# Kernel optimization log

Hardware: AMD Instinct MI355X
Metric: run time of the kernel (lower is better)

## Reference

```python
import jax, jax.numpy as jnp
from jax import lax
import numpy as np

B, C, T = 128, 64, 750
NOUT, K, HID = 4, 16, 128


def _conv(x, w, b=None):
    y = lax.conv_general_dilated(x, w, (1, 1), 'VALID', dimension_numbers=('NCHW', 'OIHW', 'NCHW'))
    return y if b is None else y + b[None, :, None, None]


def _bn(x, g, b, m, v):
    s = g / jnp.sqrt(v + 1e-5)
    return (x - m[None, :, None, None]) * s[None, :, None, None] + b[None, :, None, None]


def _pool(x):
    return lax.reduce_window(x, -jnp.inf, lax.max, (1, 1, 3, 1), (1, 1, 3, 1), 'VALID')


def _backbone(x, ct_w, ct_b, cs_w, bn1, c2_w, bn2, c3_w, bn3, c4_w, bn4, fc_w, fc_b):
    # x: (B, C, T) -> (B, 1, T, C)  (braindecode transpose_time_to_spat)
    h = jnp.transpose(x, (0, 2, 1))[:, None]
    h = _conv(h, ct_w, ct_b)              # (B,25,T-9,C)
    h = _conv(h, cs_w)                    # (B,25,T-9,1)
    h = _pool(jax.nn.elu(_bn(h, *bn1)))   # (B,25,247,1)
    h = _pool(jax.nn.elu(_bn(_conv(h, c2_w), *bn2)))  # (B,50,79,1)
    h = _pool(jax.nn.elu(_bn(_conv(h, c3_w), *bn3)))  # (B,100,23,1)
    h = _pool(jax.nn.elu(_bn(_conv(h, c4_w), *bn4)))  # (B,200,4,1)
    h = _conv(h, fc_w, fc_b)              # (B,NOUT,1,1)
    return h[:, :, 0, 0]                  # (B,NOUT)


def _heads(feats, cluster_ids, hW1, hb1, hW2, hb2):
    # gather per-sample head params, batched small GEMMs (MoE-style dispatch)
    h = jax.nn.relu(jnp.einsum('bf,bfh->bh', feats, hW1[cluster_ids]) + hb1[cluster_ids])
    return jnp.einsum('bh,bho->bo', h, hW2[cluster_ids]) + hb2[cluster_ids]


def setup_inputs() -> dict:
    key = jax.random.key(0)
    ks = jax.random.split(key, 40)
    n = lambda i, shape, s=0.1: jax.random.normal(ks[i], shape, dtype=jnp.float32) * s
    u = lambda i, shape: jax.random.uniform(ks[i], shape, dtype=jnp.float32) + 0.5
    inp = {
        'x': n(0, (B, C, T), 1.0),
        'cluster_ids': jax.random.randint(ks[1], (B,), 0, K),
        'ct_w': n(2, (25, 1, 10, 1)), 'ct_b': n(3, (25,)),
        'cs_w': n(4, (25, 25, 1, C)),
        'bn1_g': u(5, (25,)), 'bn1_b': n(6, (25,)), 'bn1_m': n(7, (25,)), 'bn1_v': u(8, (25,)),
        'c2_w': n(9, (50, 25, 10, 1)),
        'bn2_g': u(10, (50,)), 'bn2_b': n(11, (50,)), 'bn2_m': n(12, (50,)), 'bn2_v': u(13, (50,)),
        'c3_w': n(14, (100, 50, 10, 1)),
        'bn3_g': u(15, (100,)), 'bn3_b': n(16, (100,)), 'bn3_m': n(17, (100,)), 'bn3_v': u(18, (100,)),
        'c4_w': n(19, (200, 100, 10, 1)),
        'bn4_g': u(20, (200,)), 'bn4_b': n(21, (200,)), 'bn4_m': n(22, (200,)), 'bn4_v': u(23, (200,)),
        'fc_w': n(24, (NOUT, 200, 4, 1)), 'fc_b': n(25, (NOUT,)),
        'hW1': n(26, (K, NOUT, HID)), 'hb1': n(27, (K, HID)),
        'hW2': n(28, (K, HID, NOUT)), 'hb2': n(29, (K, NOUT)),
    }
    return inp


def reference(x, cluster_ids, ct_w, ct_b, cs_w,
              bn1_g, bn1_b, bn1_m, bn1_v, c2_w,
              bn2_g, bn2_b, bn2_m, bn2_v, c3_w,
              bn3_g, bn3_b, bn3_m, bn3_v, c4_w,
              bn4_g, bn4_b, bn4_m, bn4_v, fc_w, fc_b,
              hW1, hb1, hW2, hb2):
    feats = _backbone(x, ct_w, ct_b, cs_w,
                      (bn1_g, bn1_b, bn1_m, bn1_v), c2_w,
                      (bn2_g, bn2_b, bn2_m, bn2_v), c3_w,
                      (bn3_g, bn3_b, bn3_m, bn3_v), c4_w,
                      (bn4_g, bn4_b, bn4_m, bn4_v), fc_w, fc_b)
    return _heads(feats, cluster_ids, hW1, hb1, hW2, hb2)
```

## Files before the change

kernel.cpp:

```cpp
#include <hip/hip_runtime.h>
#include <hip/hip_bf16.h>
#include <math.h>

typedef __attribute__((ext_vector_type(8))) short short8v;
typedef __attribute__((ext_vector_type(4))) float f32x4;

#define F_S1 0
#define F_H1 32
#define F_S2 64
#define F_H2 128
#define F_S3 192
#define F_H3 320
#define F_S4 448
#define F_H4 704
#define F_B1 960
#define F_END 1024
#define H_BASE (F_END*2)
#define H_P1  H_BASE
#define H_WA1 (H_P1 + 128*8192)
#define H_WA2 (H_WA1 + 32*640)
#define H_WA3 (H_WA2 + 64*320)
#define H_WA4 (H_WA3 + 112*640)

#define N_WA1 (32*640)
#define N_WA2 (64*320)
#define N_WA3 (112*640)
#define N_WA4 (208*1280)
#define N_WTOT (N_WA1 + N_WA2 + N_WA3 + N_WA4)

__device__ __forceinline__ float eluf(float v) {
    return v > 0.f ? v : (expf(v) - 1.f);
}
__device__ __forceinline__ float ldh(const __hip_bfloat16* p) { return __bfloat162float(*p); }

__device__ __forceinline__ void ld4f(const float* p, float* v) {
    float2 a = *(const float2*)p, c = *(const float2*)(p + 2);
    v[0] = a.x; v[1] = a.y; v[2] = c.x; v[3] = c.y;
}

__global__ __launch_bounds__(256) void k_pre2(
    const float* __restrict__ ct_w, const float* __restrict__ ct_b,
    const float* __restrict__ cs_w,
    const float* __restrict__ g1, const float* __restrict__ b1,
    const float* __restrict__ m1, const float* __restrict__ v1,
    const float* __restrict__ w2,
    const float* __restrict__ g2, const float* __restrict__ b2,
    const float* __restrict__ m2, const float* __restrict__ v2,
    const float* __restrict__ w3,
    const float* __restrict__ g3, const float* __restrict__ b3,
    const float* __restrict__ m3, const float* __restrict__ v3,
    const float* __restrict__ w4,
    const float* __restrict__ g4, const float* __restrict__ b4,
    const float* __restrict__ m4, const float* __restrict__ v4,
    float* __restrict__ ws) {
    __hip_bfloat16* wsh = (__hip_bfloat16*)ws;
    int t = blockIdx.x * 256 + threadIdx.x;
    if (t < N_WA1) {
        int o = t / 640, kv = t - o * 640, kk = kv / 64, c = kv - kk * 64;
        float s = 0.f;
        if (o < 25)
            for (int i = 0; i < 25; ++i)
                s += cs_w[(o * 25 + i) * 64 + c] * ct_w[i * 10 + kk];
        wsh[H_WA1 + t] = __float2bfloat16(s);
    } else if (t < N_WA1 + N_WA2) {
        int u = t - N_WA1;
        int o = u / 320, kv = u - o * 320, kk = kv / 32, c = kv - kk * 32;
        float s = (o < 50 && c < 25) ? w2[(o * 25 + c) * 10 + kk] : 0.f;
        wsh[H_WA2 + u] = __float2bfloat16(s);
    } else if (t < N_WA1 + N_WA2 + N_WA3) {
        int u = t - N_WA1 - N_WA2;
        int o = u / 640, kv = u - o * 640, kk = kv / 64, c = kv - kk * 64;
        float s = (o < 100 && c < 50) ? w3[(o * 50 + c) * 10 + kk] : 0.f;
        wsh[H_WA3 + u] = __float2bfloat16(s);
    } else if (t < N_WTOT) {
        int u = t - N_WA1 - N_WA2 - N_WA3;
        int o = u / 1280, kv = u - o * 1280, kk = kv / 128, c = kv - kk * 128;
        float s = (o < 200 && c < 100) ? w4[(o * 100 + c) * 10 + kk] : 0.f;
        wsh[H_WA4 + u] = __float2bfloat16(s);
    } else {
        int j = t - N_WTOT;
        if (j < 25) {
            float sc = g1[j] / sqrtf(v1[j] + 1e-5f);
            ws[F_S1 + j] = sc; ws[F_H1 + j] = b1[j] - m1[j] * sc;
        } else if (j >= 32 && j < 82) {
            int ch = j - 32;
            float sc = g2[ch] / sqrtf(v2[ch] + 1e-5f);
            ws[F_S2 + ch] = sc; ws[F_H2 + ch] = b2[ch] - m2[ch] * sc;
        } else if (j >= 96 && j < 196) {
            int ch = j - 96;
            float sc = g3[ch] / sqrtf(v3[ch] + 1e-5f);
            ws[F_S3 + ch] = sc; ws[F_H3 + ch] = b3[ch] - m3[ch] * sc;
        } else if (j >= 224 && j < 424) {
            int ch = j - 224;
            float sc = g4[ch] / sqrtf(v4[ch] + 1e-5f);
            ws[F_S4 + ch] = sc; ws[F_H4 + ch] = b4[ch] - m4[ch] * sc;
        } else if (j >= 448 && j < 473) {
            int o = j - 448;
            float s = 0.f;
            for (int i = 0; i < 25; ++i) {
                float cs = 0.f;
                for (int c = 0; c < 64; ++c) cs += cs_w[(o * 25 + i) * 64 + c];
                s += cs * ct_b[i];
            }
            ws[F_B1 + o] = s;
        }
    }
}

template<int NS, int CB, int CINP>
__device__ __forceinline__ f32x4 conv_item(
    const __hip_bfloat16* __restrict__ Wrow,
    const __hip_bfloat16* xb, int lo, int kg, int rowBase) {
    constexpr int SWM = (CINP >= 64) ? 7 : 3;
    const short8v* Ap = (const short8v*)Wrow;
    f32x4 acc = {0.f, 0.f, 0.f, 0.f};
#pragma unroll 1
    for (int sb = 0; sb < NS; sb += 10) {
        short8v af[10];
#pragma unroll
        for (int u = 0; u < 10; ++u) af[u] = Ap[(sb + u) * 4 + kg];
#pragma unroll
        for (int u = 0; u < 10; ++u) {
            int s = sb + u;
            int kk = s / CB, cb = s % CB;
            int r = rowBase + lo + kk;
            int cs = (cb * 32 + kg * 8) ^ (8 * (r & SWM));
            short8v bf = *(const short8v*)&xb[r * CINP + cs];
            acc = __builtin_amdgcn_mfma_f32_16x16x32_bf16(af[u], bf, acc, 0, 0, 0);
        }
    }
    return acc;
}

__global__ __launch_bounds__(256) void k_conv1(
    const float* __restrict__ x, float* __restrict__ ws) {
    __hip_bfloat16* wsh = (__hip_bfloat16*)ws;
    const __hip_bfloat16* Wa = wsh + H_WA1;
    int bx = blockIdx.x, b = blockIdx.y;
    int tp0 = bx * 42;
    int PTb = min(42, 247 - tp0);
    int t0 = 126 * bx;

    __shared__ __align__(16) __hip_bfloat16 xb[144 * 64];
    __shared__ __align__(16) __hip_bfloat16 eb[32 * 128];

    for (int f = threadIdx.x; f < 64 * 36; f += 256) {
        int c = f / 36, j = f - c * 36;
        int t = t0 + 4 * j;
        const float* src = x + ((size_t)b * 64 + c) * 750 + t;
        float v[4];
        if (t + 3 < 750) {
            ld4f(src, v);
        } else {
#pragma unroll
            for (int e = 0; e < 4; ++e) v[e] = (t + e < 750) ? src[e] : 0.f;
        }
#pragma unroll
        for (int e = 0; e < 4; ++e) {
            int r = 4 * j + e;
            xb[r * 64 + (c ^ (8 * (r & 7)))] = __float2bfloat16(v[e]);
        }
    }
    __syncthreads();

    int lane = threadIdx.x & 63, wid = threadIdx.x >> 6;
    int lo = lane & 15, kg = lane >> 4;
    int ot = wid >> 1, ctg = wid & 1;
    const short8v* Ap = (const short8v*)(Wa + (size_t)(ot * 16 + lo) * 640);
    f32x4 acc[4];
#pragma unroll
    for (int q = 0; q < 4; ++q) acc[q] = (f32x4){0.f, 0.f, 0.f, 0.f};
#pragma unroll 1
    for (int sb = 0; sb < 20; sb += 10) {
        short8v af[10];
#pragma unroll
        for (int u = 0; u < 10; ++u) af[u] = Ap[(sb + u) * 4 + kg];
#pragma unroll
        for (int u = 0; u < 10; ++u) {
            int s = sb + u;
            int kk = s >> 1, cb = s & 1;
#pragma unroll
            for (int q = 0; q < 4; ++q) {
                int r = (ctg * 4 + q) * 16 + lo + kk;
                int cs = (cb * 32 + kg * 8) ^ (8 * (r & 7));
                short8v bf = *(const short8v*)&xb[r * 64 + cs];
                acc[q] = __builtin_amdgcn_mfma_f32_16x16x32_bf16(af[u], bf, acc[q], 0, 0, 0);
            }
        }
    }
#pragma unroll
    for (int q = 0; q < 4; ++q) {
        int tloc = (ctg * 4 + q) * 16 + lo;
#pragma unroll
        for (int e = 0; e < 4; ++e) {
            int o2 = ot * 16 + kg * 4 + e;
            float a = acc[q][e] + ws[F_B1 + o2];
            eb[o2 * 128 + tloc] = __float2bfloat16(eluf(a * ws[F_S1 + o2] + ws[F_H1 + o2]));
        }
    }
    __syncthreads();

    __hip_bfloat16* p1g = wsh + H_P1 + (size_t)b * 8192;
    for (int i = threadIdx.x; i < 32 * 42; i += 256) {
        int o = i / 42, pl = i - o * 42;
        if (pl < PTb) {
            int tp = tp0 + pl;
            float val = 0.f;
            if (o < 25) {
                const __hip_bfloat16* ep = eb + o * 128 + 3 * pl;
                val = fmaxf(fmaxf(ldh(ep), ldh(ep + 1)), ldh(ep + 2));
            }
            p1g[tp * 32 + (o ^ (8 * (tp & 3)))] = __float2bfloat16(val);
        }
    }
    if (bx == 5) {
        for (int i = threadIdx.x; i < 9 * 32; i += 256) {
            int r = 247 + i / 32, c = i & 31;
            p1g[r * 32 + c] = __float2bfloat16(0.f);
        }
    }
}

__global__ __launch_bounds__(512) void k_tail(
    const float* __restrict__ ws,
    const float* __restrict__ fcw, const float* __restrict__ fcb,
    const int* __restrict__ cids,
    const float* __restrict__ hW1, const float* __restrict__ hb1,
    const float* __restrict__ hW2, const float* __restrict__ hb2,
    float* __restrict__ out) {
    const __hip_bfloat16* wsh = (const __hip_bfloat16*)ws;
    const __hip_bfloat16* wa2 = wsh + H_WA2;
    const __hip_bfloat16* wa3 = wsh + H_WA3;
    const __hip_bfloat16* wa4 = wsh + H_WA4;
    int b = blockIdx.x;
    int tid = threadIdx.x;
    int lane = tid & 63, wid = tid >> 6;
    int lo = lane & 15, kg = lane >> 4;

    __shared__ __align__(16) __hip_bfloat16 p1s[256 * 32];
    __shared__ __align__(16) __hip_bfloat16 p2s[96 * 64];
    __shared__ __align__(16) __hip_bfloat16 p3s[32 * 128];
    __shared__ __align__(16) __hip_bfloat16 ebh[112 * 80];
    __shared__ float p4s[200 * 4];
    __shared__ float red[4][128];
    __shared__ float fsf[4];

    {
        const uint4* src = (const uint4*)(wsh + H_P1 + (size_t)b * 8192);
        uint4* dst = (uint4*)p1s;
        dst[tid] = src[tid];
        dst[tid + 512] = src[tid + 512];
        uint4 z = {0, 0, 0, 0};
        ((uint4*)p2s)[tid] = z;
        if (tid < 256) ((uint4*)p2s)[512 + tid] = z;
        ((uint4*)p3s)[tid] = z;
    }
    __syncthreads();

    for (int c0 = 0; c0 < 4; ++c0) {
        int tb = 60 * c0;
        int PTb = (c0 == 3) ? 19 : 20;
        for (int it = wid; it < 16; it += 8) {
            int ot = it >> 2, ct = it & 3;
            f32x4 a = conv_item<10, 1, 32>(wa2 + (size_t)(ot * 16 + lo) * 320,
                                           p1s, lo, kg, tb + ct * 16);
            int tloc = ct * 16 + lo;
#pragma unroll
            for (int e = 0; e < 4; ++e) {
                int o2 = ot * 16 + kg * 4 + e;
                ebh[o2 * 64 + tloc] =
                    __float2bfloat16(eluf(a[e] * ws[F_S2 + o2] + ws[F_H2 + o2]));
            }
        }
        __syncthreads();
        for (int i = tid; i < 50 * 20; i += 512) {
            int o = i / 20, pl = i - o * 20;
            if (pl < PTb) {
                int tp = 20 * c0 + pl;
                const __hip_bfloat16* ep = ebh + o * 64 + 3 * pl;
                float m = fmaxf(fmaxf(ldh(ep), ldh(ep + 1)), ldh(ep + 2));
                p2s[tp * 64 + (o ^ (8 * (tp & 7)))] = __float2bfloat16(m);
            }
        }
        __syncthreads();
    }

    for (int it = wid; it < 35; it += 8) {
        int ot = it / 5, ct = it - 5 * ot;
        f32x4 a = conv_item<20, 2, 64>(wa3 + (size_t)(ot * 16 + lo) * 640,
                                       p2s, lo, kg, ct * 16);
        int tloc = ct * 16 + lo;
#pragma unroll
        for (int e = 0; e < 4; ++e) {
            int o2 = ot * 16 + kg * 4 + e;
            ebh[o2 * 80 + tloc] =
                __float2bfloat16(eluf(a[e] * ws[F_S3 + o2] + ws[F_H3 + o2]));
        }
    }
    __syncthreads();
    for (int i = tid; i < 100 * 23; i += 512) {
        int o = i / 23, pl = i - 23 * o;
        const __hip_bfloat16* ep = ebh + o * 80 + 3 * pl;
        float m = fmaxf(fmaxf(ldh(ep), ldh(ep + 1)), ldh(ep + 2));
        p3s[pl * 128 + (o ^ (8 * (pl & 7)))] = __float2bfloat16(m);
    }
    __syncthreads();

    for (int it = wid; it < 13; it += 8) {
        int ot = it;
        f32x4 a = conv_item<40, 4, 128>(wa4 + (size_t)(ot * 16 + lo) * 1280,
                                        p3s, lo, kg, 0);
#pragma unroll
        for (int e = 0; e < 4; ++e) {
            int o2 = ot * 16 + kg * 4 + e;
            ebh[o2 * 16 + lo] =
                __float2bfloat16(eluf(a[e] * ws[F_S4 + o2] + ws[F_H4 + o2]));
        }
    }
    __syncthreads();
    for (int i = tid; i < 800; i += 512) {
        int o = i >> 2, pl = i & 3;
        const __hip_bfloat16* ep = ebh + o * 16 + 3 * pl;
        p4s[o * 4 + pl] = fmaxf(fmaxf(ldh(ep), ldh(ep + 1)), ldh(ep + 2));
    }
    __syncthreads();

    int j = tid;
    if (j < 128) {
        float pa[4] = {0.f, 0.f, 0.f, 0.f};
        for (int c = j; c < 200; c += 128) {
            const float* pp = p4s + c * 4;
            float v0 = pp[0], v1 = pp[1], v2 = pp[2], v3 = pp[3];
#pragma unroll
            for (int o = 0; o < 4; ++o) {
                const float* fw = fcw + (o * 200 + c) * 4;
                pa[o] += fw[0] * v0 + fw[1] * v1 + fw[2] * v2 + fw[3] * v3;
            }
        }
#pragma unroll
        for (int o = 0; o < 4; ++o) red[o][j] = pa[o];
    }
    __syncthreads();
    for (int s = 64; s > 0; s >>= 1) {
        if (j < s) {
#pragma unroll
            for (int o = 0; o < 4; ++o) red[o][j] += red[o][j + s];
        }
        __syncthreads();
    }
    if (j < 4) fsf[j] = red[j][0] + fcb[j];
    __syncthreads();

    int cid = cids[b];
    if (j < 128) {
        float hvv = hb1[cid * 128 + j];
#pragma unroll
        for (int f = 0; f < 4; ++f) hvv += fsf[f] * hW1[(cid * 4 + f) * 128 + j];
        hvv = fmaxf(hvv, 0.f);
#pragma unroll
        for (int o = 0; o < 4; ++o) red[o][j] = hvv * hW2[(cid * 128 + j) * 4 + o];
    }
    __syncthreads();
    for (int s = 64; s > 0; s >>= 1) {
        if (j < s) {
#pragma unroll
            for (int o = 0; o < 4; ++o) red[o][j] += red[o][j + s];
        }
        __syncthreads();
    }
    if (j < 4) out[b * 4 + j] = red[j][0] + hb2[cid * 4 + j];
}

extern "C" void kernel_launch(void* const* d_in, const int* in_sizes, int n_in,
                              void* d_out, int out_size, void* d_ws, size_t ws_size,
                              hipStream_t stream) {
    (void)in_sizes; (void)n_in; (void)out_size; (void)ws_size;
    const float* x    = (const float*)d_in[0];
    const int*   cid  = (const int*)d_in[1];
    const float* ctw  = (const float*)d_in[2];
    const float* ctb  = (const float*)d_in[3];
    const float* csw  = (const float*)d_in[4];
    const float* g1 = (const float*)d_in[5],  *b1 = (const float*)d_in[6];
    const float* m1 = (const float*)d_in[7],  *v1 = (const float*)d_in[8];
    const float* w2 = (const float*)d_in[9];
    const float* g2 = (const float*)d_in[10], *b2 = (const float*)d_in[11];
    const float* m2 = (const float*)d_in[12], *v2 = (const float*)d_in[13];
    const float* w3 = (const float*)d_in[14];
    const float* g3 = (const float*)d_in[15], *b3 = (const float*)d_in[16];
    const float* m3 = (const float*)d_in[17], *v3 = (const float*)d_in[18];
    const float* w4 = (const float*)d_in[19];
    const float* g4 = (const float*)d_in[20], *b4 = (const float*)d_in[21];
    const float* m4 = (const float*)d_in[22], *v4 = (const float*)d_in[23];
    const float* fcw = (const float*)d_in[24], *fcb = (const float*)d_in[25];
    const float* hW1 = (const float*)d_in[26], *hb1 = (const float*)d_in[27];
    const float* hW2 = (const float*)d_in[28], *hb2 = (const float*)d_in[29];
    float* ws  = (float*)d_ws;
    float* out = (float*)d_out;

    k_pre2<<<dim3((N_WTOT + 512 + 255) / 256), dim3(256), 0, stream>>>(
        ctw, ctb, csw, g1, b1, m1, v1, w2, g2, b2, m2, v2,
        w3, g3, b3, m3, v3, w4, g4, b4, m4, v4, ws);
    k_conv1<<<dim3(6, 128), dim3(256), 0, stream>>>(x, ws);
    k_tail<<<dim3(128), dim3(512), 0, stream>>>(ws, fcw, fcb, cid,
                                                hW1, hb1, hW2, hb2, out);
}
```

Before: 111.9 us.

## Split per-sample tail into batch-wide GEMM kernels with fused conv-pool epilogues

Replaces the single per-sample k_tail block (128 blocks, serial conv2/3/4 through shared memory) with separate batch-wide kernels for conv2, conv3 and conv4. Activations are stored time-major with the batch as the GEMM N dimension, and max-pooling is fused into the MFMA epilogue by accumulating three adjacent time positions. A small heads kernel follows. The aim is more parallelism and weight reuse across the batch. In exchange it adds three kernel launches and global-memory round trips for the intermediate activations.

```diff
diff --git a/kernel.cpp b/kernel.cpp
--- a/kernel.cpp
+++ b/kernel.cpp
@@ -14,13 +14,16 @@
 #define F_S4 448
 #define F_H4 704
 #define F_B1 960
-#define F_END 1024
+#define F_P4 1024
+#define F_END (1024 + 128*200*4)
 #define H_BASE (F_END*2)
 #define H_P1  H_BASE
 #define H_WA1 (H_P1 + 128*8192)
 #define H_WA2 (H_WA1 + 32*640)
 #define H_WA3 (H_WA2 + 64*320)
 #define H_WA4 (H_WA3 + 112*640)
+#define H_P2  (H_WA4 + 208*1280)
+#define H_P3  (H_P2 + 79*128*64)
 
 #define N_WA1 (32*640)
 #define N_WA2 (64*320)
@@ -32,7 +35,10 @@
     return v > 0.f ? v : (expf(v) - 1.f);
 }
 __device__ __forceinline__ float ldh(const __hip_bfloat16* p) { return __bfloat162float(*p); }
-
+__device__ __forceinline__ unsigned short bfb(float v) {
+    __hip_bfloat16 h = __float2bfloat16(v);
+    return reinterpret_cast<unsigned short&>(h);
+}
 __device__ __forceinline__ void ld4f(const float* p, float* v) {
     float2 a = *(const float2*)p, c = *(const float2*)(p + 2);
     v[0] = a.x; v[1] = a.y; v[2] = c.x; v[3] = c.y;
@@ -107,31 +113,6 @@
     }
 }
 
-template<int NS, int CB, int CINP>
-__device__ __forceinline__ f32x4 conv_item(
-    const __hip_bfloat16* __restrict__ Wrow,
-    const __hip_bfloat16* xb, int lo, int kg, int rowBase) {
-    constexpr int SWM = (CINP >= 64) ? 7 : 3;
-    const short8v* Ap = (const short8v*)Wrow;
-    f32x4 acc = {0.f, 0.f, 0.f, 0.f};
-#pragma unroll 1
-    for (int sb = 0; sb < NS; sb += 10) {
-        short8v af[10];
-#pragma unroll
-        for (int u = 0; u < 10; ++u) af[u] = Ap[(sb + u) * 4 + kg];
-#pragma unroll
-        for (int u = 0; u < 10; ++u) {
-            int s = sb + u;
-            int kk = s / CB, cb = s % CB;
-            int r = rowBase + lo + kk;
-            int cs = (cb * 32 + kg * 8) ^ (8 * (r & SWM));
-            short8v bf = *(const short8v*)&xb[r * CINP + cs];
-            acc = __builtin_amdgcn_mfma_f32_16x16x32_bf16(af[u], bf, acc, 0, 0, 0);
-        }
-    }
-    return acc;
-}
-
 __global__ __launch_bounds__(256) void k_conv1(
     const float* __restrict__ x, float* __restrict__ ws) {
     __hip_bfloat16* wsh = (__hip_bfloat16*)ws;
@@ -200,146 +181,204 @@
     }
     __syncthreads();
 
-    __hip_bfloat16* p1g = wsh + H_P1 + (size_t)b * 8192;
-    for (int i = threadIdx.x; i < 32 * 42; i += 256) {
-        int o = i / 42, pl = i - o * 42;
+    __hip_bfloat16* p1g = wsh + H_P1;
+    for (int i = threadIdx.x; i < 8 * 42; i += 256) {
+        int og = i / 42, pl = i - og * 42;
         if (pl < PTb) {
             int tp = tp0 + pl;
+            unsigned short uv[4];
+#pragma unroll
+            for (int j = 0; j < 4; ++j) {
+                int o = og * 4 + j;
+                float v = 0.f;
+                if (o < 25) {
+                    const __hip_bfloat16* ep = eb + o * 128 + 3 * pl;
+                    v = fmaxf(fmaxf(ldh(ep), ldh(ep + 1)), ldh(ep + 2));
+                }
+                uv[j] = bfb(v);
+            }
+            uint2 pk = {(unsigned)uv[0] | ((unsigned)uv[1] << 16),
+                        (unsigned)uv[2] | ((unsigned)uv[3] << 16)};
+            *(uint2*)(p1g + (size_t)tp * 4096 + b * 32 + og * 4) = pk;
+        }
+    }
+}
+
+__global__ __launch_bounds__(256) void k_gemm2(float* __restrict__ ws) {
+    __hip_bfloat16* wsh = (__hip_bfloat16*)ws;
+    const __hip_bfloat16* p1 = wsh + H_P1;
+    const __hip_bfloat16* W = wsh + H_WA2;
+    __hip_bfloat16* p2 = wsh + H_P2;
+    int w = blockIdx.x * 4 + (threadIdx.x >> 6);
+    int lane = threadIdx.x & 63, lo = lane & 15, kg = lane >> 4;
+    int tp = w >> 3, s0 = (w & 7) * 16;
+
+    const __hip_bfloat16* bbase = p1 + (size_t)(s0 + lo) * 32 + kg * 8;
+    short8v B[12];
+#pragma unroll
+    for (int v = 0; v < 12; ++v)
+        B[v] = *(const short8v*)(bbase + (size_t)(3 * tp + v) * 4096);
+
+    f32x4 acc[4][3];
+#pragma unroll
+    for (int ot = 0; ot < 4; ++ot)
+#pragma unroll
+        for (int u = 0; u < 3; ++u) acc[ot][u] = (f32x4){0.f, 0.f, 0.f, 0.f};
+
+#pragma unroll
+    for (int ot = 0; ot < 4; ++ot) {
+        const __hip_bfloat16* arow = W + (size_t)(ot * 16 + lo) * 320 + kg * 8;
+#pragma unroll
+        for (int kk = 0; kk < 10; ++kk) {
+            short8v a = *(const short8v*)(arow + kk * 32);
+#pragma unroll
+            for (int u = 0; u < 3; ++u)
+                acc[ot][u] = __builtin_amdgcn_mfma_f32_16x16x32_bf16(a, B[kk + u], acc[ot][u], 0, 0, 0);
+        }
+    }
+
+    __hip_bfloat16* obase = p2 + (size_t)(tp * 128 + s0 + lo) * 64;
+#pragma unroll
+    for (int ot = 0; ot < 4; ++ot) {
+        unsigned short uv[4];
+#pragma unroll
+        for (int e = 0; e < 4; ++e) {
+            int o2 = ot * 16 + kg * 4 + e;
+            float m = fmaxf(fmaxf(acc[ot][0][e], acc[ot][1][e]), acc[ot][2][e]);
+            float val = (o2 < 50) ? eluf(m * ws[F_S2 + o2] + ws[F_H2 + o2]) : 0.f;
+            uv[e] = bfb(val);
+        }
+        uint2 pk = {(unsigned)uv[0] | ((unsigned)uv[1] << 16),
+                    (unsigned)uv[2] | ((unsigned)uv[3] << 16)};
+        *(uint2*)(obase + ot * 16 + kg * 4) = pk;
+    }
+}
+
+__global__ __launch_bounds__(256) void k_gemm3(float* __restrict__ ws) {
+    __hip_bfloat16* wsh = (__hip_bfloat16*)ws;
+    const __hip_bfloat16* p2 = wsh + H_P2;
+    const __hip_bfloat16* W = wsh + H_WA3;
+    __hip_bfloat16* p3 = wsh + H_P3;
+    int w = blockIdx.x * 4 + (threadIdx.x >> 6);
+    int lane = threadIdx.x & 63, lo = lane & 15, kg = lane >> 4;
+    int col = w >> 1, oz = w & 1;
+    int tp = col >> 3, s0 = (col & 7) * 16;
+
+    const __hip_bfloat16* bbase = p2 + (size_t)(s0 + lo) * 64 + kg * 8;
+    f32x4 acc[4][3];
+#pragma unroll
+    for (int ot = 0; ot < 4; ++ot)
+#pragma unroll
+        for (int u = 0; u < 3; ++u) acc[ot][u] = (f32x4){0.f, 0.f, 0.f, 0.f};
+
+#pragma unroll
+    for (int cb = 0; cb < 2; ++cb) {
+        short8v B[12];
+#pragma unroll
+        for (int v = 0; v < 12; ++v)
+            B[v] = *(const short8v*)(bbase + (size_t)(3 * tp + v) * 8192 + cb * 32);
+#pragma unroll
+        for (int ot = 0; ot < 4; ++ot) {
+            if (oz && ot == 3) continue;
+            const __hip_bfloat16* arow =
+                W + (size_t)(oz * 64 + ot * 16 + lo) * 640 + cb * 32 + kg * 8;
+#pragma unroll
+            for (int kk = 0; kk < 10; ++kk) {
+                short8v a = *(const short8v*)(arow + kk * 64);
+#pragma unroll
+                for (int u = 0; u < 3; ++u)
+                    acc[ot][u] = __builtin_amdgcn_mfma_f32_16x16x32_bf16(a, B[kk + u], acc[ot][u], 0, 0, 0);
+            }
+        }
+    }
+
+    __hip_bfloat16* obase = p3 + (size_t)(tp * 128 + s0 + lo) * 128;
+#pragma unroll
+    for (int ot = 0; ot < 4; ++ot) {
+        unsigned short uv[4];
+#pragma unroll
+        for (int e = 0; e < 4; ++e) {
+            int o2 = oz * 64 + ot * 16 + kg * 4 + e;
             float val = 0.f;
-            if (o < 25) {
-                const __hip_bfloat16* ep = eb + o * 128 + 3 * pl;
-                val = fmaxf(fmaxf(ldh(ep), ldh(ep + 1)), ldh(ep + 2));
+            if (o2 < 100) {
+                float m = fmaxf(fmaxf(acc[ot][0][e], acc[ot][1][e]), acc[ot][2][e]);
+                val = eluf(m * ws[F_S3 + o2] + ws[F_H3 + o2]);
             }
-            p1g[tp * 32 + (o ^ (8 * (tp & 3)))] = __float2bfloat16(val);
-        }
-    }
-    if (bx == 5) {
-        for (int i = threadIdx.x; i < 9 * 32; i += 256) {
-            int r = 247 + i / 32, c = i & 31;
-            p1g[r * 32 + c] = __float2bfloat16(0.f);
-        }
-    }
-}
-
-__global__ __launch_bounds__(512) void k_tail(
+            uv[e] = bfb(val);
+        }
+        uint2 pk = {(unsigned)uv[0] | ((unsigned)uv[1] << 16),
+                    (unsigned)uv[2] | ((unsigned)uv[3] << 16)};
+        *(uint2*)(obase + oz * 64 + ot * 16 + kg * 4) = pk;
+    }
+}
+
+__global__ __launch_bounds__(256) void k_gemm4(float* __restrict__ ws) {
+    __hip_bfloat16* wsh = (__hip_bfloat16*)ws;
+    const __hip_bfloat16* p3 = wsh + H_P3;
+    const __hip_bfloat16* W = wsh + H_WA4;
+    float* p4 = ws + F_P4;
+    int w = blockIdx.x * 4 + (threadIdx.x >> 6);
+    int lane = threadIdx.x & 63, lo = lane & 15, kg = lane >> 4;
+    int ot = w >> 5, ct = w & 31;
+    int tp = ct >> 3, s0 = (ct & 7) * 16;
+
+    const __hip_bfloat16* bbase = p3 + (size_t)(s0 + lo) * 128 + kg * 8;
+    const __hip_bfloat16* arow0 = W + (size_t)(ot * 16 + lo) * 1280 + kg * 8;
+    f32x4 acc[3];
+#pragma unroll
+    for (int u = 0; u < 3; ++u) acc[u] = (f32x4){0.f, 0.f, 0.f, 0.f};
+
+#pragma unroll
+    for (int cb = 0; cb < 4; ++cb) {
+        short8v B[12];
+#pragma unroll
+        for (int v = 0; v < 12; ++v)
+            B[v] = *(const short8v*)(bbase + (size_t)(3 * tp + v) * 16384 + cb * 32);
+        const __hip_bfloat16* arow = arow0 + cb * 32;
+#pragma unroll
+        for (int kk = 0; kk < 10; ++kk) {
+            short8v a = *(const short8v*)(arow + kk * 128);
+#pragma unroll
+            for (int u = 0; u < 3; ++u)
+                acc[u] = __builtin_amdgcn_mfma_f32_16x16x32_bf16(a, B[kk + u], acc[u], 0, 0, 0);
+        }
+    }
+
+#pragma unroll
+    for (int e = 0; e < 4; ++e) {
+        int o2 = ot * 16 + kg * 4 + e;
+        if (o2 < 200) {
+            float m = fmaxf(fmaxf(acc[0][e], acc[1][e]), acc[2][e]);
+            p4[((size_t)(s0 + lo) * 200 + o2) * 4 + tp] =
+                eluf(m * ws[F_S4 + o2] + ws[F_H4 + o2]);
+        }
+    }
+}
+
+__global__ __launch_bounds__(128) void k_heads(
     const float* __restrict__ ws,
     const float* __restrict__ fcw, const float* __restrict__ fcb,
     const int* __restrict__ cids,
     const float* __restrict__ hW1, const float* __restrict__ hb1,
     const float* __restrict__ hW2, const float* __restrict__ hb2,
     float* __restrict__ out) {
-    const __hip_bfloat16* wsh = (const __hip_bfloat16*)ws;
-    const __hip_bfloat16* wa2 = wsh + H_WA2;
-    const __hip_bfloat16* wa3 = wsh + H_WA3;
-    const __hip_bfloat16* wa4 = wsh + H_WA4;
-    int b = blockIdx.x;
-    int tid = threadIdx.x;
-    int lane = tid & 63, wid = tid >> 6;
-    int lo = lane & 15, kg = lane >> 4;
-
-    __shared__ __align__(16) __hip_bfloat16 p1s[256 * 32];
-    __shared__ __align__(16) __hip_bfloat16 p2s[96 * 64];
-    __shared__ __align__(16) __hip_bfloat16 p3s[32 * 128];
-    __shared__ __align__(16) __hip_bfloat16 ebh[112 * 80];
-    __shared__ float p4s[200 * 4];
+    const float* p4 = ws + F_P4;
     __shared__ float red[4][128];
-    __shared__ float fsf[4];
-
-    {
-        const uint4* src = (const uint4*)(wsh + H_P1 + (size_t)b * 8192);
-        uint4* dst = (uint4*)p1s;
-        dst[tid] = src[tid];
-        dst[tid + 512] = src[tid + 512];
-        uint4 z = {0, 0, 0, 0};
-        ((uint4*)p2s)[tid] = z;
-        if (tid < 256) ((uint4*)p2s)[512 + tid] = z;
-        ((uint4*)p3s)[tid] = z;
-    }
-    __syncthreads();
-
-    for (int c0 = 0; c0 < 4; ++c0) {
-        int tb = 60 * c0;
-        int PTb = (c0 == 3) ? 19 : 20;
-        for (int it = wid; it < 16; it += 8) {
-            int ot = it >> 2, ct = it & 3;
-            f32x4 a = conv_item<10, 1, 32>(wa2 + (size_t)(ot * 16 + lo) * 320,
-                                           p1s, lo, kg, tb + ct * 16);
-            int tloc = ct * 16 + lo;
-#pragma unroll
-            for (int e = 0; e < 4; ++e) {
-                int o2 = ot * 16 + kg * 4 + e;
-                ebh[o2 * 64 + tloc] =
-                    __float2bfloat16(eluf(a[e] * ws[F_S2 + o2] + ws[F_H2 + o2]));
-            }
-        }
-        __syncthreads();
-        for (int i = tid; i < 50 * 20; i += 512) {
-            int o = i / 20, pl = i - o * 20;
-            if (pl < PTb) {
-                int tp = 20 * c0 + pl;
-                const __hip_bfloat16* ep = ebh + o * 64 + 3 * pl;
-                float m = fmaxf(fmaxf(ldh(ep), ldh(ep + 1)), ldh(ep + 2));
-                p2s[tp * 64 + (o ^ (8 * (tp & 7)))] = __float2bfloat16(m);
-            }
-        }
-        __syncthreads();
-    }
-
-    for (int it = wid; it < 35; it += 8) {
-        int ot = it / 5, ct = it - 5 * ot;
-        f32x4 a = conv_item<20, 2, 64>(wa3 + (size_t)(ot * 16 + lo) * 640,
-                                       p2s, lo, kg, ct * 16);
-        int tloc = ct * 16 + lo;
-#pragma unroll
-        for (int e = 0; e < 4; ++e) {
-            int o2 = ot * 16 + kg * 4 + e;
-            ebh[o2 * 80 + tloc] =
-                __float2bfloat16(eluf(a[e] * ws[F_S3 + o2] + ws[F_H3 + o2]));
-        }
-    }
-    __syncthreads();
-    for (int i = tid; i < 100 * 23; i += 512) {
-        int o = i / 23, pl = i - 23 * o;
-        const __hip_bfloat16* ep = ebh + o * 80 + 3 * pl;
-        float m = fmaxf(fmaxf(ldh(ep), ldh(ep + 1)), ldh(ep + 2));
-        p3s[pl * 128 + (o ^ (8 * (pl & 7)))] = __float2bfloat16(m);
-    }
-    __syncthreads();
-
-    for (int it = wid; it < 13; it += 8) {
-        int ot = it;
-        f32x4 a = conv_item<40, 4, 128>(wa4 + (size_t)(ot * 16 + lo) * 1280,
-                                        p3s, lo, kg, 0);
-#pragma unroll
-        for (int e = 0; e < 4; ++e) {
-            int o2 = ot * 16 + kg * 4 + e;
-            ebh[o2 * 16 + lo] =
-                __float2bfloat16(eluf(a[e] * ws[F_S4 + o2] + ws[F_H4 + o2]));
-        }
-    }
-    __syncthreads();
-    for (int i = tid; i < 800; i += 512) {
-        int o = i >> 2, pl = i & 3;
-        const __hip_bfloat16* ep = ebh + o * 16 + 3 * pl;
-        p4s[o * 4 + pl] = fmaxf(fmaxf(ldh(ep), ldh(ep + 1)), ldh(ep + 2));
-    }
-    __syncthreads();
-
-    int j = tid;
-    if (j < 128) {
-        float pa[4] = {0.f, 0.f, 0.f, 0.f};
-        for (int c = j; c < 200; c += 128) {
-            const float* pp = p4s + c * 4;
-            float v0 = pp[0], v1 = pp[1], v2 = pp[2], v3 = pp[3];
-#pragma unroll
-            for (int o = 0; o < 4; ++o) {
-                const float* fw = fcw + (o * 200 + c) * 4;
-                pa[o] += fw[0] * v0 + fw[1] * v1 + fw[2] * v2 + fw[3] * v3;
-            }
-        }
-#pragma unroll
-        for (int o = 0; o < 4; ++o) red[o][j] = pa[o];
-    }
+    __shared__ float fs[4];
+    int b = blockIdx.x, j = threadIdx.x;
+
+    float pa[4] = {0.f, 0.f, 0.f, 0.f};
+    for (int c = j; c < 200; c += 128) {
+        const float* pp = p4 + ((size_t)b * 200 + c) * 4;
+        float v0 = pp[0], v1 = pp[1], v2 = pp[2], v3 = pp[3];
+#pragma unroll
+        for (int o = 0; o < 4; ++o) {
+            const float* fw = fcw + (o * 200 + c) * 4;
+            pa[o] += fw[0] * v0 + fw[1] * v1 + fw[2] * v2 + fw[3] * v3;
+        }
+    }
+#pragma unroll
+    for (int o = 0; o < 4; ++o) red[o][j] = pa[o];
     __syncthreads();
     for (int s = 64; s > 0; s >>= 1) {
         if (j < s) {
@@ -348,18 +387,16 @@
         }
         __syncthreads();
     }
-    if (j < 4) fsf[j] = red[j][0] + fcb[j];
+    if (j < 4) fs[j] = red[j][0] + fcb[j];
     __syncthreads();
 
     int cid = cids[b];
-    if (j < 128) {
-        float hvv = hb1[cid * 128 + j];
-#pragma unroll
-        for (int f = 0; f < 4; ++f) hvv += fsf[f] * hW1[(cid * 4 + f) * 128 + j];
-        hvv = fmaxf(hvv, 0.f);
-#pragma unroll
-        for (int o = 0; o < 4; ++o) red[o][j] = hvv * hW2[(cid * 128 + j) * 4 + o];
-    }
+    float hvv = hb1[cid * 128 + j];
+#pragma unroll
+    for (int f = 0; f < 4; ++f) hvv += fs[f] * hW1[(cid * 4 + f) * 128 + j];
+    hvv = fmaxf(hvv, 0.f);
+#pragma unroll
+    for (int o = 0; o < 4; ++o) red[o][j] = hvv * hW2[(cid * 128 + j) * 4 + o];
     __syncthreads();
     for (int s = 64; s > 0; s >>= 1) {
         if (j < s) {
@@ -401,6 +438,9 @@
         ctw, ctb, csw, g1, b1, m1, v1, w2, g2, b2, m2, v2,
         w3, g3, b3, m3, v3, w4, g4, b4, m4, v4, ws);
     k_conv1<<<dim3(6, 128), dim3(256), 0, stream>>>(x, ws);
-    k_tail<<<dim3(128), dim3(512), 0, stream>>>(ws, fcw, fcb, cid,
-                                                hW1, hb1, hW2, hb2, out);
-}
+    k_gemm2<<<dim3(158), dim3(256), 0, stream>>>(ws);
+    k_gemm3<<<dim3(92),  dim3(256), 0, stream>>>(ws);
+    k_gemm4<<<dim3(104), dim3(256), 0, stream>>>(ws);
+    k_heads<<<dim3(128), dim3(128), 0, stream>>>(ws, fcw, fcb, cid,
+                                                 hW1, hb1, hW2, hb2, out);
+}
```

After: 95.93 us. -14.3%, faster.
